# Kernel tuning notes

Measured on AMD Instinct MI355X. Metric: run time of the kernel, lower is better.

## Reference

```python
import jax, jax.numpy as jnp
import numpy as np

N, E = 8192, 65536
IN_C, OUT_C, EF = 64, 16, 8
L1, L2 = 48, 32  # in - floor((in-out)/3), in - floor(2*(in-out)/3)


def setup_inputs() -> dict:
    key = jax.random.key(0)
    ks = jax.random.split(key, 10)
    rn = lambda k, shape, s: jax.random.normal(k, shape, dtype=jnp.float32) * s
    return {
        "x": jax.random.normal(ks[0], (N, IN_C), dtype=jnp.float32),
        "edge_index": jax.random.randint(ks[1], (2, E), 0, N, dtype=jnp.int32),
        "edge_attr": jax.random.normal(ks[2], (E, EF), dtype=jnp.float32),
        "nn1_w": rn(ks[3], (EF, IN_C * L1), 0.05),
        "nn1_b": jnp.zeros((IN_C * L1,), jnp.float32),
        "root1": rn(ks[4], (IN_C, L1), 0.1),
        "bias1": jnp.zeros((L1,), jnp.float32),
        "nn2_w": rn(ks[5], (EF, L1 * L2), 0.05),
        "nn2_b": jnp.zeros((L1 * L2,), jnp.float32),
        "root2": rn(ks[6], (L1, L2), 0.1),
        "bias2": jnp.zeros((L2,), jnp.float32),
        "mu_w": rn(ks[7], (L2, OUT_C), 0.1),
        "mu_b": jnp.zeros((OUT_C,), jnp.float32),
        "ls_w": rn(ks[8], (L2, OUT_C), 0.1),
        "ls_b": jnp.zeros((OUT_C,), jnp.float32),
    }


def _nnconv(x, src, dst, edge_attr, nn_w, nn_b, root, bias, c_in, c_out):
    # edge MLP -> per-edge weight matrices [E, c_in, c_out]
    w = (edge_attr @ nn_w + nn_b).reshape(-1, c_in, c_out)
    msg = jnp.einsum('ei,eio->eo', x[src], w)  # gather + per-edge matvec
    agg = jax.ops.segment_sum(msg, dst, num_segments=x.shape[0])  # sum aggregation
    return agg + x @ root + bias  # root transform + bias


def _gcn(x, src, dst, w, b):
    n = x.shape[0]
    # degree over target nodes, including self-loop (edge_weight = 1)
    deg = jax.ops.segment_sum(jnp.ones_like(src, jnp.float32), dst, num_segments=n) + 1.0
    dinv = jax.lax.rsqrt(deg)
    h = x @ w
    norm = dinv[src] * dinv[dst]  # [E]
    agg = jax.ops.segment_sum(h[src] * norm[:, None], dst, num_segments=n)
    return agg + h * (1.0 / deg)[:, None] + b  # self-loop contribution: deg_i^{-1}


def reference(x, edge_index, edge_attr, nn1_w, nn1_b, root1, bias1,
              nn2_w, nn2_b, root2, bias2, mu_w, mu_b, ls_w, ls_b):
    src, dst = edge_index[0], edge_index[1]
    h = jax.nn.relu(_nnconv(x, src, dst, edge_attr, nn1_w, nn1_b, root1, bias1, IN_C, L1))
    h = jax.nn.relu(_nnconv(h, src, dst, edge_attr, nn2_w, nn2_b, root2, bias2, L1, L2))
    return (_gcn(h, src, dst, mu_w, mu_b), _gcn(h, src, dst, ls_w, ls_b))
```

## Files before the change

kernel.cpp:

```cpp
#include <hip/hip_runtime.h>

#define NN 8192
#define EE 65536
#define IN_C 64
#define L1C 48
#define L2C 32
#define OUT_C 16
#define EF 8

#define T1_COLS 480
#define T2_COLS 320

__global__ __launch_bounds__(256) void k_T1(const float* __restrict__ x,
                                            const float* __restrict__ w,
                                            const float* __restrict__ b,
                                            const float* __restrict__ root,
                                            float* __restrict__ T1) {
    __shared__ float xsT[64 * 16];
    const int n0 = blockIdx.x * 16;
    for (int t = threadIdx.x; t < 16 * 64; t += 256) {
        int n = t >> 6, i = t & 63;
        xsT[i * 16 + n] = x[(n0 + n) * 64 + i];
    }
    __syncthreads();
    for (int c = threadIdx.x; c < T1_COLS; c += 256) {
        int f = c / 48, o = c - f * 48;
        const float* wp;
        if (f < 8)      wp = w + f * 3072 + o;
        else if (f == 8) wp = b + o;
        else             wp = root + o;
        float acc[16];
#pragma unroll
        for (int n = 0; n < 16; n++) acc[n] = 0.f;
#pragma unroll 16
        for (int i = 0; i < 64; i++) {
            float wv = wp[i * 48];
            const float* xr = &xsT[i * 16];
#pragma unroll
            for (int n = 0; n < 16; n++) acc[n] += xr[n] * wv;
        }
#pragma unroll
        for (int n = 0; n < 16; n++) T1[(size_t)(n0 + n) * T1_COLS + c] = acc[n];
    }
}

__global__ __launch_bounds__(256) void k_T2(const float* __restrict__ h1,
                                            const float* __restrict__ w,
                                            const float* __restrict__ b,
                                            const float* __restrict__ root,
                                            float* __restrict__ T2) {
    __shared__ float xsT[48 * 16];
    const int n0 = blockIdx.x * 16;
    for (int t = threadIdx.x; t < 16 * 48; t += 256) {
        int n = t / 48, i = t - n * 48;
        xsT[i * 16 + n] = h1[(n0 + n) * 48 + i];
    }
    __syncthreads();
    for (int c = threadIdx.x; c < T2_COLS; c += 256) {
        int f = c >> 5, o = c & 31;
        const float* wp;
        if (f < 8)      wp = w + f * 1536 + o;
        else if (f == 8) wp = b + o;
        else             wp = root + o;
        float acc[16];
#pragma unroll
        for (int n = 0; n < 16; n++) acc[n] = 0.f;
#pragma unroll 16
        for (int i = 0; i < 48; i++) {
            float wv = wp[i * 32];
            const float* xr = &xsT[i * 16];
#pragma unroll
            for (int n = 0; n < 16; n++) acc[n] += xr[n] * wv;
        }
#pragma unroll
        for (int n = 0; n < 16; n++) T2[(size_t)(n0 + n) * T2_COLS + c] = acc[n];
    }
}

__global__ __launch_bounds__(256) void k_zero(float* __restrict__ p, int n4) {
    int i = blockIdx.x * 256 + threadIdx.x;
    if (i < n4) ((float4*)p)[i] = make_float4(0.f, 0.f, 0.f, 0.f);
}

__global__ __launch_bounds__(256) void k_edge1(const int* __restrict__ ei,
                                               const float* __restrict__ ea,
                                               const float* __restrict__ T1,
                                               float* __restrict__ agg1) {
    int idx = blockIdx.x * 256 + threadIdx.x;
    int e = idx / 48, o = idx - e * 48;
    if (e >= EE) return;
    int s = ei[e], d = ei[EE + e];
    const float* t = T1 + (size_t)s * T1_COLS + o;
    const float4* a4 = (const float4*)(ea + (size_t)e * 8);
    float4 a0 = a4[0], a1 = a4[1];
    float m = t[384];
    m += a0.x * t[0 * 48];
    m += a0.y * t[1 * 48];
    m += a0.z * t[2 * 48];
    m += a0.w * t[3 * 48];
    m += a1.x * t[4 * 48];
    m += a1.y * t[5 * 48];
    m += a1.z * t[6 * 48];
    m += a1.w * t[7 * 48];
    atomicAdd(agg1 + (size_t)d * 48 + o, m);
}

__global__ __launch_bounds__(256) void k_h1(const float* __restrict__ agg1,
                                            const float* __restrict__ T1,
                                            const float* __restrict__ bias1,
                                            float* __restrict__ h1) {
    int idx = blockIdx.x * 256 + threadIdx.x;
    if (idx >= NN * 48) return;
    int n = idx / 48, o = idx - n * 48;
    float v = agg1[idx] + T1[(size_t)n * T1_COLS + 432 + o] + bias1[o];
    h1[idx] = v > 0.f ? v : 0.f;
}

__global__ __launch_bounds__(256) void k_edge2(const int* __restrict__ ei,
                                               const float* __restrict__ ea,
                                               const float* __restrict__ T2,
                                               float* __restrict__ agg2,
                                               float* __restrict__ deg) {
    int idx = blockIdx.x * 256 + threadIdx.x;
    int e = idx >> 5, o = idx & 31;
    if (e >= EE) return;
    int s = ei[e], d = ei[EE + e];
    const float* t = T2 + (size_t)s * T2_COLS + o;
    const float4* a4 = (const float4*)(ea + (size_t)e * 8);
    float4 a0 = a4[0], a1 = a4[1];
    float m = t[256];
    m += a0.x * t[0 * 32];
    m += a0.y * t[1 * 32];
    m += a0.z * t[2 * 32];
    m += a0.w * t[3 * 32];
    m += a1.x * t[4 * 32];
    m += a1.y * t[5 * 32];
    m += a1.z * t[6 * 32];
    m += a1.w * t[7 * 32];
    atomicAdd(agg2 + (size_t)d * 32 + o, m);
    if (o == 0) atomicAdd(deg + d, 1.0f);
}

__global__ __launch_bounds__(256) void k_post(const float* __restrict__ agg2,
                                              const float* __restrict__ T2,
                                              const float* __restrict__ bias2,
                                              const float* __restrict__ mu_w,
                                              const float* __restrict__ mu_b,
                                              const float* __restrict__ ls_w,
                                              const float* __restrict__ ls_b,
                                              const float* __restrict__ deg,
                                              float* __restrict__ hmu,
                                              float* __restrict__ hls,
                                              float* __restrict__ dinv,
                                              float* __restrict__ out) {
    __shared__ float h2s[8][32];
    const int n0 = blockIdx.x * 8;
    const int lid = threadIdx.x >> 5;
    const int o = threadIdx.x & 31;
    const int n = n0 + lid;
    float v = agg2[(size_t)n * 32 + o] + T2[(size_t)n * T2_COLS + 288 + o] + bias2[o];
    v = v > 0.f ? v : 0.f;
    h2s[lid][o] = v;
    __syncthreads();
    const float* wm = (o < 16) ? mu_w : ls_w;
    const float* bb = (o < 16) ? mu_b : ls_b;
    const int oo = o & 15;
    float acc = 0.f;
#pragma unroll
    for (int i = 0; i < 32; i++) acc += h2s[lid][i] * wm[i * 16 + oo];
    float d = deg[n] + 1.0f;
    float di = rsqrtf(d);
    if (o == 0) dinv[n] = di;
    float init = acc / d + bb[oo];
    if (o < 16) {
        hmu[(size_t)n * 16 + oo] = acc;
        out[(size_t)n * 16 + oo] = init;
    } else {
        hls[(size_t)n * 16 + oo] = acc;
        out[(size_t)NN * 16 + (size_t)n * 16 + oo] = init;
    }
}

__global__ __launch_bounds__(256) void k_gcn_edge(const int* __restrict__ ei,
                                                  const float* __restrict__ hmu,
                                                  const float* __restrict__ hls,
                                                  const float* __restrict__ dinv,
                                                  float* __restrict__ out) {
    int idx = blockIdx.x * 256 + threadIdx.x;
    int e = idx >> 4, o = idx & 15;
    if (e >= EE) return;
    int s = ei[e], d = ei[EE + e];
    float norm = dinv[s] * dinv[d];
    atomicAdd(out + (size_t)d * 16 + o, hmu[(size_t)s * 16 + o] * norm);
    atomicAdd(out + (size_t)NN * 16 + (size_t)d * 16 + o, hls[(size_t)s * 16 + o] * norm);
}

extern "C" void kernel_launch(void* const* d_in, const int* in_sizes, int n_in,
                              void* d_out, int out_size, void* d_ws, size_t ws_size,
                              hipStream_t stream) {
    const float* x     = (const float*)d_in[0];
    const int*   ei    = (const int*)d_in[1];
    const float* ea    = (const float*)d_in[2];
    const float* nn1_w = (const float*)d_in[3];
    const float* nn1_b = (const float*)d_in[4];
    const float* root1 = (const float*)d_in[5];
    const float* bias1 = (const float*)d_in[6];
    const float* nn2_w = (const float*)d_in[7];
    const float* nn2_b = (const float*)d_in[8];
    const float* root2 = (const float*)d_in[9];
    const float* bias2 = (const float*)d_in[10];
    const float* mu_w  = (const float*)d_in[11];
    const float* mu_b  = (const float*)d_in[12];
    const float* ls_w  = (const float*)d_in[13];
    const float* ls_b  = (const float*)d_in[14];
    float* out = (float*)d_out;

    float* W    = (float*)d_ws;
    float* T1   = W;
    float* T2   = W;
    float* agg1 = W + 3932160;
    float* agg2 = agg1 + 393216;
    float* deg  = agg2 + 262144;
    float* h1   = deg + 8192;
    float* hmu  = h1 + 393216;
    float* hls  = hmu + 131072;
    float* dinv = hls + 131072;

    k_T1<<<dim3(NN / 16), dim3(256), 0, stream>>>(x, nn1_w, nn1_b, root1, T1);
    k_zero<<<dim3((165888 + 255) / 256), dim3(256), 0, stream>>>(agg1, 165888);
    k_edge1<<<dim3((EE * 48) / 256), dim3(256), 0, stream>>>(ei, ea, T1, agg1);
    k_h1<<<dim3((NN * 48) / 256), dim3(256), 0, stream>>>(agg1, T1, bias1, h1);
    k_T2<<<dim3(NN / 16), dim3(256), 0, stream>>>(h1, nn2_w, nn2_b, root2, T2);
    k_edge2<<<dim3((EE * 32) / 256), dim3(256), 0, stream>>>(ei, ea, T2, agg2, deg);
    k_post<<<dim3(NN / 8), dim3(256), 0, stream>>>(agg2, T2, bias2, mu_w, mu_b,
                                                   ls_w, ls_b, deg, hmu, hls, dinv, out);
    k_gcn_edge<<<dim3((EE * 16) / 256), dim3(256), 0, stream>>>(ei, hmu, hls, dinv, out);
}
```

Baseline: 157.4 us.

## Replace atomic scatter aggregation with CSR-by-destination pull aggregation

Builds a destination-sorted CSR (count, single-block scan, atomic scatter of source and edge ids) on each call, then computes every aggregation as a per-node pull loop instead of per-edge float atomics. The relu/bias epilogues are fused into the aggregation kernels, degree comes from row lengths, and the agg buffers and their zeroing are dropped. This removes heavy atomic traffic and several launches, at the cost of CSR build overhead, a serial single-block scan, and load imbalance from variable node degrees.

```diff
diff --git a/kernel.cpp b/kernel.cpp
--- a/kernel.cpp
+++ b/kernel.cpp
@@ -82,73 +82,93 @@
     if (i < n4) ((float4*)p)[i] = make_float4(0.f, 0.f, 0.f, 0.f);
 }
 
-__global__ __launch_bounds__(256) void k_edge1(const int* __restrict__ ei,
-                                               const float* __restrict__ ea,
-                                               const float* __restrict__ T1,
-                                               float* __restrict__ agg1) {
+__global__ __launch_bounds__(256) void k_count(const int* __restrict__ ei,
+                                               int* __restrict__ cnt) {
+    int e = blockIdx.x * 256 + threadIdx.x;
+    if (e < EE) atomicAdd(&cnt[ei[EE + e]], 1);
+}
+
+__global__ __launch_bounds__(256) void k_scan(const int* __restrict__ cnt,
+                                              int* __restrict__ rowstart,
+                                              int* __restrict__ cursor) {
+    __shared__ int part[256];
+    const int t = threadIdx.x;
+    const int base = t * 32;
+    int local[32];
+    int sum = 0;
+#pragma unroll
+    for (int k = 0; k < 32; k++) { local[k] = cnt[base + k]; sum += local[k]; }
+    part[t] = sum;
+    __syncthreads();
+    if (t == 0) {
+        int run = 0;
+        for (int i = 0; i < 256; i++) { int c = part[i]; part[i] = run; run += c; }
+    }
+    __syncthreads();
+    int run = part[t];
+#pragma unroll
+    for (int k = 0; k < 32; k++) {
+        rowstart[base + k] = run;
+        cursor[base + k] = run;
+        run += local[k];
+    }
+    if (t == 255) rowstart[8192] = run;
+}
+
+__global__ __launch_bounds__(256) void k_scatter(const int* __restrict__ ei,
+                                                 int* __restrict__ cursor,
+                                                 int* __restrict__ ssrc,
+                                                 int* __restrict__ seid) {
+    int e = blockIdx.x * 256 + threadIdx.x;
+    if (e >= EE) return;
+    int d = ei[EE + e];
+    int pos = atomicAdd(&cursor[d], 1);
+    ssrc[pos] = ei[e];
+    seid[pos] = e;
+}
+
+__global__ __launch_bounds__(256) void k_agg1(const int* __restrict__ rowstart,
+                                              const int* __restrict__ ssrc,
+                                              const int* __restrict__ seid,
+                                              const float* __restrict__ ea,
+                                              const float* __restrict__ T1,
+                                              const float* __restrict__ bias1,
+                                              float* __restrict__ h1) {
     int idx = blockIdx.x * 256 + threadIdx.x;
-    int e = idx / 48, o = idx - e * 48;
-    if (e >= EE) return;
-    int s = ei[e], d = ei[EE + e];
-    const float* t = T1 + (size_t)s * T1_COLS + o;
-    const float4* a4 = (const float4*)(ea + (size_t)e * 8);
-    float4 a0 = a4[0], a1 = a4[1];
-    float m = t[384];
-    m += a0.x * t[0 * 48];
-    m += a0.y * t[1 * 48];
-    m += a0.z * t[2 * 48];
-    m += a0.w * t[3 * 48];
-    m += a1.x * t[4 * 48];
-    m += a1.y * t[5 * 48];
-    m += a1.z * t[6 * 48];
-    m += a1.w * t[7 * 48];
-    atomicAdd(agg1 + (size_t)d * 48 + o, m);
-}
-
-__global__ __launch_bounds__(256) void k_h1(const float* __restrict__ agg1,
-                                            const float* __restrict__ T1,
-                                            const float* __restrict__ bias1,
-                                            float* __restrict__ h1) {
-    int idx = blockIdx.x * 256 + threadIdx.x;
-    if (idx >= NN * 48) return;
     int n = idx / 48, o = idx - n * 48;
-    float v = agg1[idx] + T1[(size_t)n * T1_COLS + 432 + o] + bias1[o];
-    h1[idx] = v > 0.f ? v : 0.f;
-}
-
-__global__ __launch_bounds__(256) void k_edge2(const int* __restrict__ ei,
-                                               const float* __restrict__ ea,
-                                               const float* __restrict__ T2,
-                                               float* __restrict__ agg2,
-                                               float* __restrict__ deg) {
-    int idx = blockIdx.x * 256 + threadIdx.x;
-    int e = idx >> 5, o = idx & 31;
-    if (e >= EE) return;
-    int s = ei[e], d = ei[EE + e];
-    const float* t = T2 + (size_t)s * T2_COLS + o;
-    const float4* a4 = (const float4*)(ea + (size_t)e * 8);
-    float4 a0 = a4[0], a1 = a4[1];
-    float m = t[256];
-    m += a0.x * t[0 * 32];
-    m += a0.y * t[1 * 32];
-    m += a0.z * t[2 * 32];
-    m += a0.w * t[3 * 32];
-    m += a1.x * t[4 * 32];
-    m += a1.y * t[5 * 32];
-    m += a1.z * t[6 * 32];
-    m += a1.w * t[7 * 32];
-    atomicAdd(agg2 + (size_t)d * 32 + o, m);
-    if (o == 0) atomicAdd(deg + d, 1.0f);
-}
-
-__global__ __launch_bounds__(256) void k_post(const float* __restrict__ agg2,
+    if (n >= NN) return;
+    const int rs = rowstart[n], re = rowstart[n + 1];
+    float m = 0.f;
+    for (int j = rs; j < re; ++j) {
+        int s = ssrc[j], eid = seid[j];
+        const float* t = T1 + (size_t)s * T1_COLS + o;
+        const float4* a4 = (const float4*)(ea + (size_t)eid * 8);
+        float4 a0 = a4[0], a1 = a4[1];
+        float acc = t[384];
+        acc += a0.x * t[0 * 48];
+        acc += a0.y * t[1 * 48];
+        acc += a0.z * t[2 * 48];
+        acc += a0.w * t[3 * 48];
+        acc += a1.x * t[4 * 48];
+        acc += a1.y * t[5 * 48];
+        acc += a1.z * t[6 * 48];
+        acc += a1.w * t[7 * 48];
+        m += acc;
+    }
+    float v = m + T1[(size_t)n * T1_COLS + 432 + o] + bias1[o];
+    h1[(size_t)n * 48 + o] = v > 0.f ? v : 0.f;
+}
+
+__global__ __launch_bounds__(256) void k_agg2(const int* __restrict__ rowstart,
+                                              const int* __restrict__ ssrc,
+                                              const int* __restrict__ seid,
+                                              const float* __restrict__ ea,
                                               const float* __restrict__ T2,
                                               const float* __restrict__ bias2,
                                               const float* __restrict__ mu_w,
                                               const float* __restrict__ mu_b,
                                               const float* __restrict__ ls_w,
                                               const float* __restrict__ ls_b,
-                                              const float* __restrict__ deg,
                                               float* __restrict__ hmu,
                                               float* __restrict__ hls,
                                               float* __restrict__ dinv,
@@ -158,9 +178,26 @@
     const int lid = threadIdx.x >> 5;
     const int o = threadIdx.x & 31;
     const int n = n0 + lid;
-    float v = agg2[(size_t)n * 32 + o] + T2[(size_t)n * T2_COLS + 288 + o] + bias2[o];
-    v = v > 0.f ? v : 0.f;
-    h2s[lid][o] = v;
+    const int rs = rowstart[n], re = rowstart[n + 1];
+    float m = 0.f;
+    for (int j = rs; j < re; ++j) {
+        int s = ssrc[j], eid = seid[j];
+        const float* t = T2 + (size_t)s * T2_COLS + o;
+        const float4* a4 = (const float4*)(ea + (size_t)eid * 8);
+        float4 a0 = a4[0], a1 = a4[1];
+        float acc = t[256];
+        acc += a0.x * t[0 * 32];
+        acc += a0.y * t[1 * 32];
+        acc += a0.z * t[2 * 32];
+        acc += a0.w * t[3 * 32];
+        acc += a1.x * t[4 * 32];
+        acc += a1.y * t[5 * 32];
+        acc += a1.z * t[6 * 32];
+        acc += a1.w * t[7 * 32];
+        m += acc;
+    }
+    float v = m + T2[(size_t)n * T2_COLS + 288 + o] + bias2[o];
+    h2s[lid][o] = v > 0.f ? v : 0.f;
     __syncthreads();
     const float* wm = (o < 16) ? mu_w : ls_w;
     const float* bb = (o < 16) ? mu_b : ls_b;
@@ -168,7 +205,7 @@
     float acc = 0.f;
 #pragma unroll
     for (int i = 0; i < 32; i++) acc += h2s[lid][i] * wm[i * 16 + oo];
-    float d = deg[n] + 1.0f;
+    float d = (float)(re - rs) + 1.0f;
     float di = rsqrtf(d);
     if (o == 0) dinv[n] = di;
     float init = acc / d + bb[oo];
@@ -181,18 +218,26 @@
     }
 }
 
-__global__ __launch_bounds__(256) void k_gcn_edge(const int* __restrict__ ei,
-                                                  const float* __restrict__ hmu,
-                                                  const float* __restrict__ hls,
-                                                  const float* __restrict__ dinv,
-                                                  float* __restrict__ out) {
+__global__ __launch_bounds__(256) void k_gcn(const int* __restrict__ rowstart,
+                                             const int* __restrict__ ssrc,
+                                             const float* __restrict__ hmu,
+                                             const float* __restrict__ hls,
+                                             const float* __restrict__ dinv,
+                                             float* __restrict__ out) {
     int idx = blockIdx.x * 256 + threadIdx.x;
-    int e = idx >> 4, o = idx & 15;
-    if (e >= EE) return;
-    int s = ei[e], d = ei[EE + e];
-    float norm = dinv[s] * dinv[d];
-    atomicAdd(out + (size_t)d * 16 + o, hmu[(size_t)s * 16 + o] * norm);
-    atomicAdd(out + (size_t)NN * 16 + (size_t)d * 16 + o, hls[(size_t)s * 16 + o] * norm);
+    int d = idx >> 4, o = idx & 15;
+    if (d >= NN) return;
+    const int rs = rowstart[d], re = rowstart[d + 1];
+    float accm = 0.f, accl = 0.f;
+    for (int j = rs; j < re; ++j) {
+        int s = ssrc[j];
+        float ds_ = dinv[s];
+        accm += hmu[(size_t)s * 16 + o] * ds_;
+        accl += hls[(size_t)s * 16 + o] * ds_;
+    }
+    float did = dinv[d];
+    out[(size_t)d * 16 + o] += accm * did;
+    out[(size_t)NN * 16 + (size_t)d * 16 + o] += accl * did;
 }
 
 extern "C" void kernel_launch(void* const* d_in, const int* in_sizes, int n_in,
@@ -218,21 +263,27 @@
     float* W    = (float*)d_ws;
     float* T1   = W;
     float* T2   = W;
-    float* agg1 = W + 3932160;
-    float* agg2 = agg1 + 393216;
-    float* deg  = agg2 + 262144;
-    float* h1   = deg + 8192;
+    float* h1   = W + 3932160;
     float* hmu  = h1 + 393216;
     float* hls  = hmu + 131072;
     float* dinv = hls + 131072;
-
+    int* cnt      = (int*)(dinv + 8192);
+    int* rowstart = cnt + 8192;
+    int* cursor   = rowstart + 8193;
+    int* ssrc     = cursor + 8192;
+    int* seid     = ssrc + 65536;
+
+    k_zero<<<dim3(8), dim3(256), 0, stream>>>((float*)cnt, 2048);
+    k_count<<<dim3(EE / 256), dim3(256), 0, stream>>>(ei, cnt);
     k_T1<<<dim3(NN / 16), dim3(256), 0, stream>>>(x, nn1_w, nn1_b, root1, T1);
-    k_zero<<<dim3((165888 + 255) / 256), dim3(256), 0, stream>>>(agg1, 165888);
-    k_edge1<<<dim3((EE * 48) / 256), dim3(256), 0, stream>>>(ei, ea, T1, agg1);
-    k_h1<<<dim3((NN * 48) / 256), dim3(256), 0, stream>>>(agg1, T1, bias1, h1);
+    k_scan<<<dim3(1), dim3(256), 0, stream>>>(cnt, rowstart, cursor);
+    k_scatter<<<dim3(EE / 256), dim3(256), 0, stream>>>(ei, cursor, ssrc, seid);
+    k_agg1<<<dim3((NN * 48 + 255) / 256), dim3(256), 0, stream>>>(
+        rowstart, ssrc, seid, ea, T1, bias1, h1);
     k_T2<<<dim3(NN / 16), dim3(256), 0, stream>>>(h1, nn2_w, nn2_b, root2, T2);
-    k_edge2<<<dim3((EE * 32) / 256), dim3(256), 0, stream>>>(ei, ea, T2, agg2, deg);
-    k_post<<<dim3(NN / 8), dim3(256), 0, stream>>>(agg2, T2, bias2, mu_w, mu_b,
-                                                   ls_w, ls_b, deg, hmu, hls, dinv, out);
-    k_gcn_edge<<<dim3((EE * 16) / 256), dim3(256), 0, stream>>>(ei, hmu, hls, dinv, out);
-}
+    k_agg2<<<dim3(NN / 8), dim3(256), 0, stream>>>(
+        rowstart, ssrc, seid, ea, T2, bias2, mu_w, mu_b, ls_w, ls_b,
+        hmu, hls, dinv, out);
+    k_gcn<<<dim3((NN * 16) / 256), dim3(256), 0, stream>>>(
+        rowstart, ssrc, hmu, hls, dinv, out);
+}
```

After: 175.2 us. 1.11x slower.

## Sort edges by source node to improve gather locality in edge kernels

Applied to the files above, without the earlier changes.

Adds a counting sort of edges by source node (count, single-block scan, atomic scatter) that builds permuted src/dst/edge_attr arrays. All three edge kernels then walk edges in source order, so consecutive edges reuse the same T1/T2/h rows in cache. The in-degree is now an integer count from the count kernel, which removes the float degree atomics from edge2. The cost is three extra small launches, including a serial single-block scan, plus the scatter traffic. Because the sort uses an atomic cursor, edge order within a bucket is nondeterministic, which can change float summation order.

```diff
diff --git a/kernel.cpp b/kernel.cpp
--- a/kernel.cpp
+++ b/kernel.cpp
@@ -82,16 +82,69 @@
     if (i < n4) ((float4*)p)[i] = make_float4(0.f, 0.f, 0.f, 0.f);
 }
 
-__global__ __launch_bounds__(256) void k_edge1(const int* __restrict__ ei,
-                                               const float* __restrict__ ea,
+__global__ __launch_bounds__(256) void k_count(const int* __restrict__ ei,
+                                               int* __restrict__ cnt_src,
+                                               int* __restrict__ cnt_dst) {
+    int e = blockIdx.x * 256 + threadIdx.x;
+    if (e < EE) {
+        atomicAdd(&cnt_src[ei[e]], 1);
+        atomicAdd(&cnt_dst[ei[EE + e]], 1);
+    }
+}
+
+__global__ __launch_bounds__(256) void k_scan(const int* __restrict__ cnt,
+                                              int* __restrict__ cursor) {
+    __shared__ int part[256];
+    const int t = threadIdx.x;
+    const int base = t * 32;
+    int local[32];
+    int sum = 0;
+#pragma unroll
+    for (int k = 0; k < 32; k++) { local[k] = cnt[base + k]; sum += local[k]; }
+    part[t] = sum;
+    __syncthreads();
+    if (t == 0) {
+        int run = 0;
+        for (int i = 0; i < 256; i++) { int c = part[i]; part[i] = run; run += c; }
+    }
+    __syncthreads();
+    int run = part[t];
+#pragma unroll
+    for (int k = 0; k < 32; k++) {
+        cursor[base + k] = run;
+        run += local[k];
+    }
+}
+
+__global__ __launch_bounds__(256) void k_scatter(const int* __restrict__ ei,
+                                                 const float* __restrict__ ea,
+                                                 int* __restrict__ cursor,
+                                                 int* __restrict__ ssrc,
+                                                 int* __restrict__ sdst,
+                                                 float* __restrict__ sea) {
+    int e = blockIdx.x * 256 + threadIdx.x;
+    if (e >= EE) return;
+    int s = ei[e], d = ei[EE + e];
+    int pos = atomicAdd(&cursor[s], 1);
+    ssrc[pos] = s;
+    sdst[pos] = d;
+    const float4* a = (const float4*)(ea + (size_t)e * 8);
+    float4* bp = (float4*)(sea + (size_t)pos * 8);
+    bp[0] = a[0];
+    bp[1] = a[1];
+}
+
+__global__ __launch_bounds__(256) void k_edge1(const int* __restrict__ ssrc,
+                                               const int* __restrict__ sdst,
+                                               const float* __restrict__ sea,
                                                const float* __restrict__ T1,
                                                float* __restrict__ agg1) {
     int idx = blockIdx.x * 256 + threadIdx.x;
-    int e = idx / 48, o = idx - e * 48;
-    if (e >= EE) return;
-    int s = ei[e], d = ei[EE + e];
+    int j = idx / 48, o = idx - j * 48;
+    if (j >= EE) return;
+    int s = ssrc[j], d = sdst[j];
     const float* t = T1 + (size_t)s * T1_COLS + o;
-    const float4* a4 = (const float4*)(ea + (size_t)e * 8);
+    const float4* a4 = (const float4*)(sea + (size_t)j * 8);
     float4 a0 = a4[0], a1 = a4[1];
     float m = t[384];
     m += a0.x * t[0 * 48];
@@ -116,17 +169,17 @@
     h1[idx] = v > 0.f ? v : 0.f;
 }
 
-__global__ __launch_bounds__(256) void k_edge2(const int* __restrict__ ei,
-                                               const float* __restrict__ ea,
+__global__ __launch_bounds__(256) void k_edge2(const int* __restrict__ ssrc,
+                                               const int* __restrict__ sdst,
+                                               const float* __restrict__ sea,
                                                const float* __restrict__ T2,
-                                               float* __restrict__ agg2,
-                                               float* __restrict__ deg) {
-    int idx = blockIdx.x * 256 + threadIdx.x;
-    int e = idx >> 5, o = idx & 31;
-    if (e >= EE) return;
-    int s = ei[e], d = ei[EE + e];
+                                               float* __restrict__ agg2) {
+    int idx = blockIdx.x * 256 + threadIdx.x;
+    int j = idx >> 5, o = idx & 31;
+    if (j >= EE) return;
+    int s = ssrc[j], d = sdst[j];
     const float* t = T2 + (size_t)s * T2_COLS + o;
-    const float4* a4 = (const float4*)(ea + (size_t)e * 8);
+    const float4* a4 = (const float4*)(sea + (size_t)j * 8);
     float4 a0 = a4[0], a1 = a4[1];
     float m = t[256];
     m += a0.x * t[0 * 32];
@@ -138,7 +191,6 @@
     m += a1.z * t[6 * 32];
     m += a1.w * t[7 * 32];
     atomicAdd(agg2 + (size_t)d * 32 + o, m);
-    if (o == 0) atomicAdd(deg + d, 1.0f);
 }
 
 __global__ __launch_bounds__(256) void k_post(const float* __restrict__ agg2,
@@ -148,7 +200,7 @@
                                               const float* __restrict__ mu_b,
                                               const float* __restrict__ ls_w,
                                               const float* __restrict__ ls_b,
-                                              const float* __restrict__ deg,
+                                              const int* __restrict__ cnt_dst,
                                               float* __restrict__ hmu,
                                               float* __restrict__ hls,
                                               float* __restrict__ dinv,
@@ -168,7 +220,7 @@
     float acc = 0.f;
 #pragma unroll
     for (int i = 0; i < 32; i++) acc += h2s[lid][i] * wm[i * 16 + oo];
-    float d = deg[n] + 1.0f;
+    float d = (float)cnt_dst[n] + 1.0f;
     float di = rsqrtf(d);
     if (o == 0) dinv[n] = di;
     float init = acc / d + bb[oo];
@@ -181,15 +233,16 @@
     }
 }
 
-__global__ __launch_bounds__(256) void k_gcn_edge(const int* __restrict__ ei,
+__global__ __launch_bounds__(256) void k_gcn_edge(const int* __restrict__ ssrc,
+                                                  const int* __restrict__ sdst,
                                                   const float* __restrict__ hmu,
                                                   const float* __restrict__ hls,
                                                   const float* __restrict__ dinv,
                                                   float* __restrict__ out) {
     int idx = blockIdx.x * 256 + threadIdx.x;
-    int e = idx >> 4, o = idx & 15;
-    if (e >= EE) return;
-    int s = ei[e], d = ei[EE + e];
+    int j = idx >> 4, o = idx & 15;
+    if (j >= EE) return;
+    int s = ssrc[j], d = sdst[j];
     float norm = dinv[s] * dinv[d];
     atomicAdd(out + (size_t)d * 16 + o, hmu[(size_t)s * 16 + o] * norm);
     atomicAdd(out + (size_t)NN * 16 + (size_t)d * 16 + o, hls[(size_t)s * 16 + o] * norm);
@@ -220,19 +273,27 @@
     float* T2   = W;
     float* agg1 = W + 3932160;
     float* agg2 = agg1 + 393216;
-    float* deg  = agg2 + 262144;
-    float* h1   = deg + 8192;
+    int* cnt_src = (int*)(agg2 + 262144);
+    int* cnt_dst = cnt_src + 8192;
+    float* h1   = (float*)(cnt_dst + 8192);
     float* hmu  = h1 + 393216;
     float* hls  = hmu + 131072;
     float* dinv = hls + 131072;
-
+    int* cursor = (int*)(dinv + 8192);
+    int* ssrc   = cursor + 8192;
+    int* sdst   = ssrc + 65536;
+    float* sea  = (float*)(sdst + 65536);
+
+    k_zero<<<dim3(656), dim3(256), 0, stream>>>(agg1, 167936);
+    k_count<<<dim3(EE / 256), dim3(256), 0, stream>>>(ei, cnt_src, cnt_dst);
     k_T1<<<dim3(NN / 16), dim3(256), 0, stream>>>(x, nn1_w, nn1_b, root1, T1);
-    k_zero<<<dim3((165888 + 255) / 256), dim3(256), 0, stream>>>(agg1, 165888);
-    k_edge1<<<dim3((EE * 48) / 256), dim3(256), 0, stream>>>(ei, ea, T1, agg1);
+    k_scan<<<dim3(1), dim3(256), 0, stream>>>(cnt_src, cursor);
+    k_scatter<<<dim3(EE / 256), dim3(256), 0, stream>>>(ei, ea, cursor, ssrc, sdst, sea);
+    k_edge1<<<dim3((EE * 48) / 256), dim3(256), 0, stream>>>(ssrc, sdst, sea, T1, agg1);
     k_h1<<<dim3((NN * 48) / 256), dim3(256), 0, stream>>>(agg1, T1, bias1, h1);
     k_T2<<<dim3(NN / 16), dim3(256), 0, stream>>>(h1, nn2_w, nn2_b, root2, T2);
-    k_edge2<<<dim3((EE * 32) / 256), dim3(256), 0, stream>>>(ei, ea, T2, agg2, deg);
+    k_edge2<<<dim3((EE * 32) / 256), dim3(256), 0, stream>>>(ssrc, sdst, sea, T2, agg2);
     k_post<<<dim3(NN / 8), dim3(256), 0, stream>>>(agg2, T2, bias2, mu_w, mu_b,
-                                                   ls_w, ls_b, deg, hmu, hls, dinv, out);
-    k_gcn_edge<<<dim3((EE * 16) / 256), dim3(256), 0, stream>>>(ei, hmu, hls, dinv, out);
-}
+                                                   ls_w, ls_b, cnt_dst, hmu, hls, dinv, out);
+    k_gcn_edge<<<dim3((EE * 16) / 256), dim3(256), 0, stream>>>(ssrc, sdst, hmu, hls, dinv, out);
+}
```

Result: slower. 166.2 us (+5.5%).
